# Optimization experiments

Hardware: AMD Instinct MI355X
Metric: run time of the kernel (lower is better)

## Reference

```python
import jax, jax.numpy as jnp
import numpy as np

N = 50000   # nodes
E = 600000  # edges
D = 128     # input_dim == output_dim
H = 4       # heads
C = D // H  # per-head dim = 32
NEG_SLOPE = 0.2
LN_EPS = 1e-5


def setup_inputs() -> dict:
    key = jax.random.key(0)
    ks = jax.random.split(key, 6)
    s = 1.0 / np.sqrt(D)
    x = jax.random.normal(ks[0], (N, D), jnp.float32)
    edge_index = jax.random.randint(ks[1], (2, E), 0, N, dtype=jnp.int64)
    W = jax.random.normal(ks[2], (D, H * C), jnp.float32) * s          # GATConv lin (no bias)
    att_src = jax.random.normal(ks[3], (H, C), jnp.float32) * s
    att_dst = jax.random.normal(ks[4], (H, C), jnp.float32) * s
    bias = jnp.zeros((H * C,), jnp.float32)
    gamma = jnp.ones((D,), jnp.float32)   # LayerNorm weight
    beta = jnp.zeros((D,), jnp.float32)   # LayerNorm bias
    return {"x": x, "edge_index": edge_index, "W": W, "att_src": att_src,
            "att_dst": att_dst, "bias": bias, "gamma": gamma, "beta": beta}


def reference(x, edge_index, W, att_src, att_dst, bias, gamma, beta):
    n = x.shape[0]
    h = (x @ W).reshape(n, H, C)                       # [N,H,C] transformed node feats
    # PyG default add_self_loops=True
    loops = jnp.arange(n, dtype=edge_index.dtype)
    src = jnp.concatenate([edge_index[0], loops])      # message source j
    dst = jnp.concatenate([edge_index[1], loops])      # aggregation target i
    # per-node attention logits, gathered per edge
    a_src = jnp.einsum('nhc,hc->nh', h, att_src)       # [N,H]
    a_dst = jnp.einsum('nhc,hc->nh', h, att_dst)
    e = jax.nn.leaky_relu(a_src[src] + a_dst[dst], NEG_SLOPE)   # [Etot,H]
    # numerically-stable segment softmax over edges grouped by dst
    m = jax.ops.segment_max(e, dst, num_segments=n)    # every node has a self loop
    e = jnp.exp(e - m[dst])
    denom = jax.ops.segment_sum(e, dst, num_segments=n)
    alpha = e / (denom[dst] + 1e-16)                   # [Etot,H]
    # weighted scatter-add aggregation
    msg = h[src] * alpha[:, :, None]                   # [Etot,H,C]
    out = jax.ops.segment_sum(msg, dst, num_segments=n).reshape(n, H * C) + bias
    # GELU (torch default: exact erf) -> LayerNorm -> residual (dropout=identity in eval)
    f = jax.nn.gelu(out, approximate=False)
    mu = jnp.mean(f, axis=-1, keepdims=True)
    var = jnp.var(f, axis=-1, keepdims=True)
    f = (f - mu) / jnp.sqrt(var + LN_EPS) * gamma + beta
    return f + x
```

## Files before the change

kernel.cpp:

```cpp
#include <hip/hip_runtime.h>
#include <hip/hip_bf16.h>
#include <math.h>

#define DD 128
#define HH 4
#define NEG_SLOPE 0.2f
#define LN_EPS 1e-5f

typedef __attribute__((ext_vector_type(8))) short bf16x8;
typedef __attribute__((ext_vector_type(8))) unsigned short us16x8;
typedef __attribute__((ext_vector_type(4))) float f32x4;

__device__ __forceinline__ float lrelu(float e) { return fmaxf(e, NEG_SLOPE * e); }
__device__ __forceinline__ float bflo(unsigned u) { return __uint_as_float(u << 16); }
__device__ __forceinline__ float bfhi(unsigned u) { return __uint_as_float(u & 0xFFFF0000u); }
__device__ __forceinline__ unsigned short f2bf(float f) {
    return __builtin_bit_cast(unsigned short, __float2bfloat16(f));
}


__global__ __launch_bounds__(256) void wtrans(const float* __restrict__ W,
                                              unsigned short* __restrict__ WTb) {
    __shared__ float tile[16][128];
    int b = blockIdx.x;
    int t = threadIdx.x;
#pragma unroll
    for (int i = 0; i < 8; i++) {
        int flat = i * 256 + t;
        int kk = flat >> 7, colc = flat & 127;
        tile[kk][colc] = W[(b * 16 + kk) * DD + colc];
    }
    __syncthreads();
    int colc = t & 127, half = t >> 7;
    us16x8 tmp;
#pragma unroll
    for (int kk = 0; kk < 8; kk++) tmp[kk] = f2bf(tile[half * 8 + kk][colc]);
    *(uint4*)&WTb[colc * DD + b * 16 + half * 8] = __builtin_bit_cast(uint4, tmp);
}


__global__ __launch_bounds__(256) void count_kernel(const int* __restrict__ ei,
                                                    int* __restrict__ deg, int E) {
    int i = blockIdx.x * 256 + threadIdx.x;
    if (i < E) atomicAdd(&deg[ei[E + i]], 1);
}

__global__ __launch_bounds__(256) void partial_kernel(const int* __restrict__ deg,
                                                      int* __restrict__ bpart, int n) {
    __shared__ int r[4];
    int i = blockIdx.x * 256 + threadIdx.x;
    int v = (i < n) ? deg[i] : 0;
#pragma unroll
    for (int m = 1; m < 64; m <<= 1) v += __shfl_xor(v, m);
    if ((threadIdx.x & 63) == 0) r[threadIdx.x >> 6] = v;
    __syncthreads();
    if (threadIdx.x == 0) bpart[blockIdx.x] = r[0] + r[1] + r[2] + r[3];
}

__global__ __launch_bounds__(256) void scanpart_kernel(int* __restrict__ bpart, int nb) {
    int t = threadIdx.x;
    int v = (t < nb) ? bpart[t] : 0;
    __shared__ int ws[4];
    int x = v;
#pragma unroll
    for (int m = 1; m < 64; m <<= 1) {
        int y = __shfl_up(x, m);
        if ((t & 63) >= m) x += y;
    }
    if ((t & 63) == 63) ws[t >> 6] = x;
    __syncthreads();
    int add = 0;
    for (int w = 0; w < (t >> 6); w++) add += ws[w];
    x += add;
    if (t < nb) bpart[t] = x - v;
}

__global__ __launch_bounds__(256) void writeoff_kernel(const int* __restrict__ deg,
                                                       const int* __restrict__ bpart,
                                                       int* __restrict__ rowstart,
                                                       int* __restrict__ cursor, int n, int E) {
    int i = blockIdx.x * 256 + threadIdx.x;
    int t = threadIdx.x;
    int v = (i < n) ? deg[i] : 0;
    __shared__ int ws[4];
    int x = v;
#pragma unroll
    for (int m = 1; m < 64; m <<= 1) {
        int y = __shfl_up(x, m);
        if ((t & 63) >= m) x += y;
    }
    if ((t & 63) == 63) ws[t >> 6] = x;
    __syncthreads();
    int add = bpart[blockIdx.x];
    for (int w = 0; w < (t >> 6); w++) add += ws[w];
    int excl = x - v + add;
    if (i < n) { rowstart[i] = excl; cursor[i] = excl; }
    if (i == 0) rowstart[n] = E;
}

__global__ __launch_bounds__(256) void fill_kernel(const int* __restrict__ ei,
                            const float* __restrict__ aS, const float* __restrict__ aD,
                            int* __restrict__ cursor, int* __restrict__ col,
                            float* __restrict__ el, int E) {
    int i = blockIdx.x * 256 + threadIdx.x;
    if (i >= E) return;
    int s = ei[i];
    int d = ei[E + i];
    int pos = atomicAdd(&cursor[d], 1);
    col[pos] = s;
    float4 sv = ((const float4*)aS)[s];
    float4 dv = ((const float4*)aD)[d];
    float4 ev;
    ev.x = __expf(lrelu(sv.x + dv.x));
    ev.y = __expf(lrelu(sv.y + dv.y));
    ev.z = __expf(lrelu(sv.z + dv.z));
    ev.w = __expf(lrelu(sv.w + dv.w));
    ((float4*)el)[pos] = ev;
}


__global__ __launch_bounds__(256) void gemm_mfma(const float* __restrict__ X,
                                                 const unsigned short* __restrict__ WTb,
                                                 unsigned short* __restrict__ Hb, int n) {
    __shared__ unsigned short lds[DD * DD];
    int t = threadIdx.x;
    const uint4* src = (const uint4*)WTb;
#pragma unroll
    for (int i = 0; i < 8; i++) {
        int b = i * 256 + t;
        uint4 v = src[b];
        int byteaddr = b * 16;
        int col = b >> 4;
        int swz = byteaddr ^ ((col & 15) << 4);
        *(uint4*)((char*)lds + swz) = v;
    }
    __syncthreads();

    int w = t >> 6, l = t & 63;
    int R = blockIdx.x * 64 + w * 16;
    int row = R + (l & 15);
    int rclamp = min(row, n - 1);
    int q = l >> 4;

    f32x4 acc[8];
#pragma unroll
    for (int c = 0; c < 8; c++) acc[c] = (f32x4){0.f, 0.f, 0.f, 0.f};

#pragma unroll
    for (int ks = 0; ks < 4; ks++) {
        const float* ap = X + (long)rclamp * DD + ks * 32 + q * 8;
        float4 a0 = *(const float4*)ap;
        float4 a1 = *(const float4*)(ap + 4);
        bf16x8 af;
        af[0] = (short)f2bf(a0.x); af[1] = (short)f2bf(a0.y);
        af[2] = (short)f2bf(a0.z); af[3] = (short)f2bf(a0.w);
        af[4] = (short)f2bf(a1.x); af[5] = (short)f2bf(a1.y);
        af[6] = (short)f2bf(a1.z); af[7] = (short)f2bf(a1.w);
#pragma unroll
        for (int c = 0; c < 8; c++) {
            int col = c * 16 + (l & 15);
            int byteaddr = col * 256 + ks * 64 + q * 16;
            int swz = byteaddr ^ ((col & 15) << 4);
            bf16x8 bfr = *(const bf16x8*)((const char*)lds + swz);
            acc[c] = __builtin_amdgcn_mfma_f32_16x16x32_bf16(af, bfr, acc[c], 0, 0, 0);
        }
    }

    int rowbase = R + q * 4;
#pragma unroll
    for (int c = 0; c < 8; c++) {
        int colw = c * 16 + (l & 15);
#pragma unroll
        for (int r = 0; r < 4; r++) {
            int orow = rowbase + r;
            if (orow < n) Hb[(long)orow * DD + colw] = f2bf(acc[c][r]);
        }
    }
}


__global__ __launch_bounds__(256) void logits_bf16(const uint4* __restrict__ Hb4,
                                                   const float* __restrict__ attS,
                                                   const float* __restrict__ attD,
                                                   float* __restrict__ aS,
                                                   float* __restrict__ aD,
                                                   float* __restrict__ pSelf, int n) {
    long idx = (long)blockIdx.x * 256 + threadIdx.x;
    if (idx >= (long)n * 16) return;
    int seg = (int)(idx & 15);
    int node = (int)(idx >> 4);
    int c0 = seg * 8;
    uint4 v = Hb4[idx];
    unsigned u[4] = {v.x, v.y, v.z, v.w};
    float s = 0.f, d = 0.f;
#pragma unroll
    for (int i = 0; i < 4; i++) {
        float lo = bflo(u[i]), hi = bfhi(u[i]);
        s += lo * attS[c0 + 2*i] + hi * attS[c0 + 2*i + 1];
        d += lo * attD[c0 + 2*i] + hi * attD[c0 + 2*i + 1];
    }
#pragma unroll
    for (int m = 1; m < 4; m <<= 1) {
        s += __shfl_xor(s, m);
        d += __shfl_xor(d, m);
    }
    if ((seg & 3) == 0) {
        int h = seg >> 2;
        aS[node * HH + h] = s;
        aD[node * HH + h] = d;
        pSelf[node * HH + h] = __expf(lrelu(s + d));
    }
}


__global__ __launch_bounds__(256) void agg_kernel(const unsigned* __restrict__ Hb2,
                                                  const float* __restrict__ pSelf,
                                                  const float* __restrict__ el,
                                                  const int* __restrict__ rowstart,
                                                  const int* __restrict__ col,
                                                  const float* __restrict__ X,
                                                  const float* __restrict__ bias,
                                                  const float* __restrict__ gamma,
                                                  const float* __restrict__ beta,
                                                  float* __restrict__ out, int n) {
    int node = blockIdx.x * 4 + (threadIdx.x >> 6);
    if (node >= n) return;
    int lane = threadIdx.x & 63;
    int c0 = lane * 2;
    int hh = lane >> 4;

    int rs = rowstart[node];
    int re = rowstart[node + 1];

    float p = pSelf[node * HH + hh];
    unsigned hv = Hb2[(long)node * 64 + lane];
    float d0 = p, ax0 = p * bflo(hv), ay0 = p * bfhi(hv);
    float d1 = 0.f, ax1 = 0.f, ay1 = 0.f;
    float d2 = 0.f, ax2 = 0.f, ay2 = 0.f;
    float d3 = 0.f, ax3 = 0.f, ay3 = 0.f;

    int k = rs;
    for (; k + 4 <= re; k += 4) {
        int j0 = col[k], j1 = col[k + 1], j2 = col[k + 2], j3 = col[k + 3];
        float p0 = el[k * 4 + hh];
        float p1 = el[k * 4 + 4 + hh];
        float p2 = el[k * 4 + 8 + hh];
        float p3 = el[k * 4 + 12 + hh];
        unsigned g0 = Hb2[(long)j0 * 64 + lane];
        unsigned g1 = Hb2[(long)j1 * 64 + lane];
        unsigned g2 = Hb2[(long)j2 * 64 + lane];
        unsigned g3 = Hb2[(long)j3 * 64 + lane];
        d0 += p0; ax0 += p0 * bflo(g0); ay0 += p0 * bfhi(g0);
        d1 += p1; ax1 += p1 * bflo(g1); ay1 += p1 * bfhi(g1);
        d2 += p2; ax2 += p2 * bflo(g2); ay2 += p2 * bfhi(g2);
        d3 += p3; ax3 += p3 * bflo(g3); ay3 += p3 * bfhi(g3);
    }
    for (; k < re; k++) {
        int j0 = col[k];
        float p0 = el[k * 4 + hh];
        unsigned g0 = Hb2[(long)j0 * 64 + lane];
        d0 += p0; ax0 += p0 * bflo(g0); ay0 += p0 * bfhi(g0);
    }
    float denom = (d0 + d1) + (d2 + d3);
    float ax = (ax0 + ax1) + (ax2 + ax3);
    float ay = (ay0 + ay1) + (ay2 + ay3);

    float2 b2 = ((const float2*)bias)[lane];
    float inv = 1.0f / (denom + 1e-16f);
    float o0 = ax * inv + b2.x;
    float o1 = ay * inv + b2.y;
    float g0 = 0.5f * o0 * (1.0f + erff(o0 * 0.70710678118654752f));
    float g1 = 0.5f * o1 * (1.0f + erff(o1 * 0.70710678118654752f));

    float s1 = g0 + g1, s2 = g0 * g0 + g1 * g1;
#pragma unroll
    for (int msk = 1; msk < 64; msk <<= 1) {
        s1 += __shfl_xor(s1, msk);
        s2 += __shfl_xor(s2, msk);
    }
    float mean = s1 * (1.0f / 128.0f);
    float var = s2 * (1.0f / 128.0f) - mean * mean;
    float rstd = rsqrtf(var + LN_EPS);
    float2 gm2 = ((const float2*)gamma)[lane];
    float2 bt2 = ((const float2*)beta)[lane];
    float f0 = (g0 - mean) * rstd * gm2.x + bt2.x;
    float f1 = (g1 - mean) * rstd * gm2.y + bt2.y;

    float2 xv = ((const float2*)X)[(long)node * 64 + lane];
    float2 ov;
    ov.x = f0 + xv.x;
    ov.y = f1 + xv.y;
    ((float2*)out)[(long)node * 64 + lane] = ov;
}


extern "C" void kernel_launch(void* const* d_in, const int* in_sizes, int n_in,
                              void* d_out, int out_size, void* d_ws, size_t ws_size,
                              hipStream_t stream) {
    const float* x    = (const float*)d_in[0];
    const int*   ei   = (const int*)d_in[1];
    const float* W    = (const float*)d_in[2];
    const float* attS = (const float*)d_in[3];
    const float* attD = (const float*)d_in[4];
    const float* bias = (const float*)d_in[5];
    const float* gamma= (const float*)d_in[6];
    const float* beta = (const float*)d_in[7];
    float* out = (float*)d_out;

    int n = in_sizes[0] / DD;
    int E = in_sizes[1] / 2;
    int nb = (n + 255) / 256;
    int eb = (E + 255) / 256;

    char* ws = (char*)d_ws;
    size_t off = 0;
    auto alloc = [&](size_t bytes) -> void* {
        void* p = ws + off;
        off = (off + bytes + 255) & ~(size_t)255;
        return p;
    };
    unsigned short* Hb  = (unsigned short*)alloc((size_t)n * DD * 2);
    unsigned short* WTb = (unsigned short*)alloc((size_t)DD * DD * 2);
    float* aS       = (float*)alloc((size_t)n * HH * 4);
    float* aD       = (float*)alloc((size_t)n * HH * 4);
    float* pSelf    = (float*)alloc((size_t)n * HH * 4);
    int*   deg      = (int*)alloc((size_t)n * 4);
    int*   rowstart = (int*)alloc((size_t)(n + 1) * 4);
    int*   cursor   = (int*)alloc((size_t)n * 4);
    int*   col      = (int*)alloc((size_t)E * 4);
    float* el       = (float*)alloc((size_t)E * HH * 4);
    int*   bpart    = (int*)alloc((size_t)nb * 4);

    hipMemsetAsync(deg, 0, (size_t)n * 4, stream);
    wtrans<<<8, 256, 0, stream>>>(W, WTb);
    count_kernel<<<eb, 256, 0, stream>>>(ei, deg, E);
    partial_kernel<<<nb, 256, 0, stream>>>(deg, bpart, n);
    scanpart_kernel<<<1, 256, 0, stream>>>(bpart, nb);
    writeoff_kernel<<<nb, 256, 0, stream>>>(deg, bpart, rowstart, cursor, n, E);

    gemm_mfma<<<(n + 63) / 64, 256, 0, stream>>>(x, WTb, Hb, n);
    logits_bf16<<<(int)(((long)n * 16 + 255) / 256), 256, 0, stream>>>(
        (const uint4*)Hb, attS, attD, aS, aD, pSelf, n);

    fill_kernel<<<eb, 256, 0, stream>>>(ei, aS, aD, cursor, col, el, E);

    agg_kernel<<<(n + 3) / 4, 256, 0, stream>>>((const unsigned*)Hb, pSelf, el,
                                                rowstart, col, x, bias, gamma, beta, out, n);
}
```

Measured before the change: 203.7 us.

## Fuse logits into GEMM, merge CSR scan kernels, pack edge records in bf16

```diff
diff --git a/kernel.cpp b/kernel.cpp
--- a/kernel.cpp
+++ b/kernel.cpp
@@ -19,70 +19,68 @@
 }
 
 
-__global__ __launch_bounds__(256) void wtrans(const float* __restrict__ W,
-                                              unsigned short* __restrict__ WTb) {
-    __shared__ float tile[16][128];
+__global__ __launch_bounds__(256) void wtrans_zero(const float* __restrict__ W,
+                                                   unsigned short* __restrict__ WTb,
+                                                   int* __restrict__ deg,
+                                                   int* __restrict__ bpart,
+                                                   int n, int nb, int zb) {
     int b = blockIdx.x;
     int t = threadIdx.x;
-#pragma unroll
-    for (int i = 0; i < 8; i++) {
-        int flat = i * 256 + t;
-        int kk = flat >> 7, colc = flat & 127;
-        tile[kk][colc] = W[(b * 16 + kk) * DD + colc];
-    }
-    __syncthreads();
-    int colc = t & 127, half = t >> 7;
-    us16x8 tmp;
-#pragma unroll
-    for (int kk = 0; kk < 8; kk++) tmp[kk] = f2bf(tile[half * 8 + kk][colc]);
-    *(uint4*)&WTb[colc * DD + b * 16 + half * 8] = __builtin_bit_cast(uint4, tmp);
+    if (b < 8) {
+        __shared__ float tile[16][128];
+#pragma unroll
+        for (int i = 0; i < 8; i++) {
+            int flat = i * 256 + t;
+            int kk = flat >> 7, colc = flat & 127;
+            tile[kk][colc] = W[(b * 16 + kk) * DD + colc];
+        }
+        __syncthreads();
+        int colc = t & 127, half = t >> 7;
+        us16x8 tmp;
+#pragma unroll
+        for (int kk = 0; kk < 8; kk++) tmp[kk] = f2bf(tile[half * 8 + kk][colc]);
+        *(uint4*)&WTb[colc * DD + b * 16 + half * 8] = __builtin_bit_cast(uint4, tmp);
+    } else if (b < 8 + zb) {
+        int base = (b - 8) * 1024 + t;
+#pragma unroll
+        for (int i = 0; i < 4; i++) {
+            int idx = base + i * 256;
+            if (idx < n) deg[idx] = 0;
+        }
+    } else {
+        if (t < nb) bpart[t] = 0;
+    }
 }
 
 
 __global__ __launch_bounds__(256) void count_kernel(const int* __restrict__ ei,
-                                                    int* __restrict__ deg, int E) {
+                                                    int* __restrict__ deg,
+                                                    int* __restrict__ bpart, int E) {
     int i = blockIdx.x * 256 + threadIdx.x;
-    if (i < E) atomicAdd(&deg[ei[E + i]], 1);
-}
-
-__global__ __launch_bounds__(256) void partial_kernel(const int* __restrict__ deg,
-                                                      int* __restrict__ bpart, int n) {
-    __shared__ int r[4];
-    int i = blockIdx.x * 256 + threadIdx.x;
-    int v = (i < n) ? deg[i] : 0;
-#pragma unroll
-    for (int m = 1; m < 64; m <<= 1) v += __shfl_xor(v, m);
-    if ((threadIdx.x & 63) == 0) r[threadIdx.x >> 6] = v;
-    __syncthreads();
-    if (threadIdx.x == 0) bpart[blockIdx.x] = r[0] + r[1] + r[2] + r[3];
-}
-
-__global__ __launch_bounds__(256) void scanpart_kernel(int* __restrict__ bpart, int nb) {
-    int t = threadIdx.x;
-    int v = (t < nb) ? bpart[t] : 0;
-    __shared__ int ws[4];
-    int x = v;
-#pragma unroll
-    for (int m = 1; m < 64; m <<= 1) {
-        int y = __shfl_up(x, m);
-        if ((t & 63) >= m) x += y;
-    }
-    if ((t & 63) == 63) ws[t >> 6] = x;
-    __syncthreads();
-    int add = 0;
-    for (int w = 0; w < (t >> 6); w++) add += ws[w];
-    x += add;
-    if (t < nb) bpart[t] = x - v;
-}
+    if (i < E) {
+        int d = ei[E + i];
+        atomicAdd(&deg[d], 1);
+        atomicAdd(&bpart[d >> 8], 1);
+    }
+}
+
 
 __global__ __launch_bounds__(256) void writeoff_kernel(const int* __restrict__ deg,
                                                        const int* __restrict__ bpart,
                                                        int* __restrict__ rowstart,
                                                        int* __restrict__ cursor, int n, int E) {
-    int i = blockIdx.x * 256 + threadIdx.x;
+    __shared__ int addsh;
+    __shared__ int ws[4];
     int t = threadIdx.x;
+    if (t < 64) {
+        int s = 0;
+        for (int i = t; i < blockIdx.x; i += 64) s += bpart[i];
+#pragma unroll
+        for (int m = 1; m < 64; m <<= 1) s += __shfl_xor(s, m);
+        if (t == 0) addsh = s;
+    }
+    int i = blockIdx.x * 256 + t;
     int v = (i < n) ? deg[i] : 0;
-    __shared__ int ws[4];
     int x = v;
 #pragma unroll
     for (int m = 1; m < 64; m <<= 1) {
@@ -91,7 +89,7 @@
     }
     if ((t & 63) == 63) ws[t >> 6] = x;
     __syncthreads();
-    int add = bpart[blockIdx.x];
+    int add = addsh;
     for (int w = 0; w < (t >> 6); w++) add += ws[w];
     int excl = x - v + add;
     if (i < n) { rowstart[i] = excl; cursor[i] = excl; }
@@ -100,28 +98,35 @@
 
 __global__ __launch_bounds__(256) void fill_kernel(const int* __restrict__ ei,
                             const float* __restrict__ aS, const float* __restrict__ aD,
-                            int* __restrict__ cursor, int* __restrict__ col,
-                            float* __restrict__ el, int E) {
+                            int* __restrict__ cursor, uint4* __restrict__ recbuf, int E) {
     int i = blockIdx.x * 256 + threadIdx.x;
     if (i >= E) return;
     int s = ei[i];
     int d = ei[E + i];
     int pos = atomicAdd(&cursor[d], 1);
-    col[pos] = s;
     float4 sv = ((const float4*)aS)[s];
     float4 dv = ((const float4*)aD)[d];
-    float4 ev;
-    ev.x = __expf(lrelu(sv.x + dv.x));
-    ev.y = __expf(lrelu(sv.y + dv.y));
-    ev.z = __expf(lrelu(sv.z + dv.z));
-    ev.w = __expf(lrelu(sv.w + dv.w));
-    ((float4*)el)[pos] = ev;
+    float p0 = __expf(lrelu(sv.x + dv.x));
+    float p1 = __expf(lrelu(sv.y + dv.y));
+    float p2 = __expf(lrelu(sv.z + dv.z));
+    float p3 = __expf(lrelu(sv.w + dv.w));
+    uint4 rec;
+    rec.x = (unsigned)s;
+    rec.y = (unsigned)f2bf(p0) | ((unsigned)f2bf(p1) << 16);
+    rec.z = (unsigned)f2bf(p2) | ((unsigned)f2bf(p3) << 16);
+    rec.w = 0;
+    recbuf[pos] = rec;
 }
 
 
 __global__ __launch_bounds__(256) void gemm_mfma(const float* __restrict__ X,
                                                  const unsigned short* __restrict__ WTb,
-                                                 unsigned short* __restrict__ Hb, int n) {
+                                                 const float* __restrict__ attS,
+                                                 const float* __restrict__ attD,
+                                                 unsigned short* __restrict__ Hb,
+                                                 float* __restrict__ aS,
+                                                 float* __restrict__ aD,
+                                                 float* __restrict__ pSelf, int n) {
     __shared__ unsigned short lds[DD * DD];
     int t = threadIdx.x;
     const uint4* src = (const uint4*)WTb;
@@ -138,9 +143,8 @@
 
     int w = t >> 6, l = t & 63;
     int R = blockIdx.x * 64 + w * 16;
-    int row = R + (l & 15);
-    int rclamp = min(row, n - 1);
-    int q = l >> 4;
+    int l15 = l & 15, q = l >> 4;
+    int rclamp = min(R + l15, n - 1);
 
     f32x4 acc[8];
 #pragma unroll
@@ -158,7 +162,7 @@
         af[6] = (short)f2bf(a1.z); af[7] = (short)f2bf(a1.w);
 #pragma unroll
         for (int c = 0; c < 8; c++) {
-            int col = c * 16 + (l & 15);
+            int col = c * 16 + l15;
             int byteaddr = col * 256 + ks * 64 + q * 16;
             int swz = byteaddr ^ ((col & 15) << 4);
             bf16x8 bfr = *(const bf16x8*)((const char*)lds + swz);
@@ -169,55 +173,69 @@
     int rowbase = R + q * 4;
 #pragma unroll
     for (int c = 0; c < 8; c++) {
-        int colw = c * 16 + (l & 15);
+        int colw = c * 16 + l15;
 #pragma unroll
         for (int r = 0; r < 4; r++) {
             int orow = rowbase + r;
             if (orow < n) Hb[(long)orow * DD + colw] = f2bf(acc[c][r]);
         }
     }
-}
-
-
-__global__ __launch_bounds__(256) void logits_bf16(const uint4* __restrict__ Hb4,
-                                                   const float* __restrict__ attS,
-                                                   const float* __restrict__ attD,
-                                                   float* __restrict__ aS,
-                                                   float* __restrict__ aD,
-                                                   float* __restrict__ pSelf, int n) {
-    long idx = (long)blockIdx.x * 256 + threadIdx.x;
-    if (idx >= (long)n * 16) return;
-    int seg = (int)(idx & 15);
-    int node = (int)(idx >> 4);
-    int c0 = seg * 8;
-    uint4 v = Hb4[idx];
-    unsigned u[4] = {v.x, v.y, v.z, v.w};
-    float s = 0.f, d = 0.f;
-#pragma unroll
-    for (int i = 0; i < 4; i++) {
-        float lo = bflo(u[i]), hi = bfhi(u[i]);
-        s += lo * attS[c0 + 2*i] + hi * attS[c0 + 2*i + 1];
-        d += lo * attD[c0 + 2*i] + hi * attD[c0 + 2*i + 1];
-    }
-#pragma unroll
-    for (int m = 1; m < 4; m <<= 1) {
-        s += __shfl_xor(s, m);
-        d += __shfl_xor(d, m);
-    }
-    if ((seg & 3) == 0) {
-        int h = seg >> 2;
-        aS[node * HH + h] = s;
-        aD[node * HH + h] = d;
-        pSelf[node * HH + h] = __expf(lrelu(s + d));
-    }
-}
-
+
+    float attSl[8], attDl[8];
+#pragma unroll
+    for (int h = 0; h < 4; h++) {
+        attSl[2 * h]     = attS[h * 32 + l15];
+        attSl[2 * h + 1] = attS[h * 32 + 16 + l15];
+        attDl[2 * h]     = attD[h * 32 + l15];
+        attDl[2 * h + 1] = attD[h * 32 + 16 + l15];
+    }
+    float sA[4][4], sD[4][4];
+#pragma unroll
+    for (int r = 0; r < 4; r++)
+#pragma unroll
+        for (int h = 0; h < 4; h++) {
+            sA[r][h] = acc[2 * h][r] * attSl[2 * h] + acc[2 * h + 1][r] * attSl[2 * h + 1];
+            sD[r][h] = acc[2 * h][r] * attDl[2 * h] + acc[2 * h + 1][r] * attDl[2 * h + 1];
+        }
+#pragma unroll
+    for (int m = 1; m < 16; m <<= 1)
+#pragma unroll
+        for (int r = 0; r < 4; r++)
+#pragma unroll
+            for (int h = 0; h < 4; h++) {
+                sA[r][h] += __shfl_xor(sA[r][h], m);
+                sD[r][h] += __shfl_xor(sD[r][h], m);
+            }
+#pragma unroll
+    for (int r = 0; r < 4; r++) {
+        if (l15 == r) {
+            int node = rowbase + r;
+            if (node < n) {
+                float4 s4 = make_float4(sA[r][0], sA[r][1], sA[r][2], sA[r][3]);
+                float4 d4 = make_float4(sD[r][0], sD[r][1], sD[r][2], sD[r][3]);
+                float4 p4;
+                p4.x = __expf(lrelu(s4.x + d4.x));
+                p4.y = __expf(lrelu(s4.y + d4.y));
+                p4.z = __expf(lrelu(s4.z + d4.z));
+                p4.w = __expf(lrelu(s4.w + d4.w));
+                *(float4*)&aS[node * HH] = s4;
+                *(float4*)&aD[node * HH] = d4;
+                *(float4*)&pSelf[node * HH] = p4;
+            }
+        }
+    }
+}
+
+
+__device__ __forceinline__ float pe_of(uint4 r, int hh) {
+    unsigned wd = (hh & 2) ? r.z : r.y;
+    return (hh & 1) ? bfhi(wd) : bflo(wd);
+}
 
 __global__ __launch_bounds__(256) void agg_kernel(const unsigned* __restrict__ Hb2,
                                                   const float* __restrict__ pSelf,
-                                                  const float* __restrict__ el,
+                                                  const uint4* __restrict__ recbuf,
                                                   const int* __restrict__ rowstart,
-                                                  const int* __restrict__ col,
                                                   const float* __restrict__ X,
                                                   const float* __restrict__ bias,
                                                   const float* __restrict__ gamma,
@@ -226,7 +244,6 @@
     int node = blockIdx.x * 4 + (threadIdx.x >> 6);
     if (node >= n) return;
     int lane = threadIdx.x & 63;
-    int c0 = lane * 2;
     int hh = lane >> 4;
 
     int rs = rowstart[node];
@@ -241,24 +258,25 @@
 
     int k = rs;
     for (; k + 4 <= re; k += 4) {
-        int j0 = col[k], j1 = col[k + 1], j2 = col[k + 2], j3 = col[k + 3];
-        float p0 = el[k * 4 + hh];
-        float p1 = el[k * 4 + 4 + hh];
-        float p2 = el[k * 4 + 8 + hh];
-        float p3 = el[k * 4 + 12 + hh];
-        unsigned g0 = Hb2[(long)j0 * 64 + lane];
-        unsigned g1 = Hb2[(long)j1 * 64 + lane];
-        unsigned g2 = Hb2[(long)j2 * 64 + lane];
-        unsigned g3 = Hb2[(long)j3 * 64 + lane];
+        uint4 r0 = recbuf[k];
+        uint4 r1 = recbuf[k + 1];
+        uint4 r2 = recbuf[k + 2];
+        uint4 r3 = recbuf[k + 3];
+        float p0 = pe_of(r0, hh), p1 = pe_of(r1, hh);
+        float p2 = pe_of(r2, hh), p3 = pe_of(r3, hh);
+        unsigned g0 = Hb2[(long)(int)r0.x * 64 + lane];
+        unsigned g1 = Hb2[(long)(int)r1.x * 64 + lane];
+        unsigned g2 = Hb2[(long)(int)r2.x * 64 + lane];
+        unsigned g3 = Hb2[(long)(int)r3.x * 64 + lane];
         d0 += p0; ax0 += p0 * bflo(g0); ay0 += p0 * bfhi(g0);
         d1 += p1; ax1 += p1 * bflo(g1); ay1 += p1 * bfhi(g1);
         d2 += p2; ax2 += p2 * bflo(g2); ay2 += p2 * bfhi(g2);
         d3 += p3; ax3 += p3 * bflo(g3); ay3 += p3 * bfhi(g3);
     }
     for (; k < re; k++) {
-        int j0 = col[k];
-        float p0 = el[k * 4 + hh];
-        unsigned g0 = Hb2[(long)j0 * 64 + lane];
+        uint4 r0 = recbuf[k];
+        float p0 = pe_of(r0, hh);
+        unsigned g0 = Hb2[(long)(int)r0.x * 64 + lane];
         d0 += p0; ax0 += p0 * bflo(g0); ay0 += p0 * bfhi(g0);
     }
     float denom = (d0 + d1) + (d2 + d3);
@@ -311,6 +329,7 @@
     int E = in_sizes[1] / 2;
     int nb = (n + 255) / 256;
     int eb = (E + 255) / 256;
+    int zb = (n + 1023) / 1024;
 
     char* ws = (char*)d_ws;
     size_t off = 0;
@@ -327,23 +346,17 @@
     int*   deg      = (int*)alloc((size_t)n * 4);
     int*   rowstart = (int*)alloc((size_t)(n + 1) * 4);
     int*   cursor   = (int*)alloc((size_t)n * 4);
-    int*   col      = (int*)alloc((size_t)E * 4);
-    float* el       = (float*)alloc((size_t)E * HH * 4);
+    uint4* rec      = (uint4*)alloc((size_t)E * 16);
     int*   bpart    = (int*)alloc((size_t)nb * 4);
 
-    hipMemsetAsync(deg, 0, (size_t)n * 4, stream);
-    wtrans<<<8, 256, 0, stream>>>(W, WTb);
-    count_kernel<<<eb, 256, 0, stream>>>(ei, deg, E);
-    partial_kernel<<<nb, 256, 0, stream>>>(deg, bpart, n);
-    scanpart_kernel<<<1, 256, 0, stream>>>(bpart, nb);
+    wtrans_zero<<<8 + zb + 1, 256, 0, stream>>>(W, WTb, deg, bpart, n, nb, zb);
+    count_kernel<<<eb, 256, 0, stream>>>(ei, deg, bpart, E);
     writeoff_kernel<<<nb, 256, 0, stream>>>(deg, bpart, rowstart, cursor, n, E);
 
-    gemm_mfma<<<(n + 63) / 64, 256, 0, stream>>>(x, WTb, Hb, n);
-    logits_bf16<<<(int)(((long)n * 16 + 255) / 256), 256, 0, stream>>>(
-        (const uint4*)Hb, attS, attD, aS, aD, pSelf, n);
-
-    fill_kernel<<<eb, 256, 0, stream>>>(ei, aS, aD, cursor, col, el, E);
-
-    agg_kernel<<<(n + 3) / 4, 256, 0, stream>>>((const unsigned*)Hb, pSelf, el,
-                                                rowstart, col, x, bias, gamma, beta, out, n);
-}
+    gemm_mfma<<<(n + 63) / 64, 256, 0, stream>>>(x, WTb, attS, attD, Hb, aS, aD, pSelf, n);
+
+    fill_kernel<<<eb, 256, 0, stream>>>(ei, aS, aD, cursor, rec, E);
+
+    agg_kernel<<<(n + 3) / 4, 256, 0, stream>>>((const unsigned*)Hb, pSelf, rec,
+                                                rowstart, x, bias, gamma, beta, out, n);
+}
```

Result: slower. 535.4 us (+162.8%).
